# Kernel tuning notes

Hardware: AMD Instinct MI355X
Metric: run time of the kernel (lower is better)

Reference implementation:

```python
import jax, jax.numpy as jnp
import numpy as np

B, N, C, H = 4, 1024, 1024, 16
D = C // H  # head_dim = 64
SCALE = D ** -0.5


def setup_inputs() -> dict:
    key = jax.random.key(0)
    ks = jax.random.split(key, 7)
    std = 0.02
    return {
        "xq": jax.random.normal(ks[0], (B, N, C), dtype=jnp.float32),
        "xk": jax.random.normal(ks[1], (B, N, C), dtype=jnp.float32),
        "xv": jax.random.normal(ks[2], (B, N, C), dtype=jnp.float32),
        # torch nn.Linear weights are [out_features, in_features]
        "Wq": jax.random.normal(ks[3], (C, C), dtype=jnp.float32) * std,
        "Wkv": jax.random.normal(ks[4], (2 * C, C), dtype=jnp.float32) * std,
        "Wp": jax.random.normal(ks[5], (C, C), dtype=jnp.float32) * std,
        "bp": jax.random.normal(ks[6], (C,), dtype=jnp.float32) * std,
    }


def reference(xq, xk, xv, Wq, Wkv, Wp, bp):
    b, nq, c = xq.shape
    nk = xk.shape[1]
    # q projection -> [B, H, Nq, D]
    q = (xq @ Wq.T).reshape(b, nq, H, D).transpose(0, 2, 1, 3)
    # HPA: shared projection produces K and V from xk (xv unused)
    kv = xk @ Wkv.T  # [B, Nk, 2C]
    k, v = jnp.split(kv, 2, axis=-1)
    k = k.reshape(b, nk, H, D).transpose(0, 2, 1, 3)  # [B, H, Nk, D]
    v = v.reshape(b, nk, H, D).transpose(0, 2, 1, 3)  # [B, H, Nk, D]
    # pre-softmax scores (attn_save in original)
    attn = jnp.einsum("bhqd,bhkd->bhqk", q, k) * SCALE  # [B, H, Nq, Nk]
    p = jax.nn.softmax(attn, axis=-1)
    x = jnp.einsum("bhqk,bhkd->bhqd", p, v)  # [B, H, Nq, D]
    x = x.transpose(0, 2, 1, 3).reshape(b, nq, c)
    x = x @ Wp.T + bp
    # returns (x transposed to [Nq, B, C], mean-over-heads pre-softmax scores)
    return x.transpose(1, 0, 2), attn.sum(axis=1) / H
```

## Files before the change

kernel.cpp:

```cpp
#include <hip/hip_runtime.h>
#include <hip/hip_bf16.h>
#include <stdint.h>

typedef __attribute__((ext_vector_type(8))) short bf16x8;
typedef __attribute__((ext_vector_type(4))) float f32x4;

#define B_DIM 4
#define N_DIM 1024
#define C_DIM 1024
#define NT 16

#define QSCALE 0.18033688011112042f
#define OUT1_ALPHA 0.04332169878499658f

__device__ __forceinline__ ushort f2bf(float f) {
  union { float f; uint32_t u; } v; v.f = f;
  uint32_t r = (v.u + 0x7FFFu + ((v.u >> 16) & 1u)) >> 16;
  return (ushort)r;
}

__device__ __forceinline__ uint32_t cvtpk(float lo, float hi) {
  uint32_t r;
  asm("v_cvt_pk_bf16_f32 %0, %1, %2" : "=v"(r) : "v"(lo), "v"(hi));
  return r;
}

__device__ __forceinline__ void gload_lds16(const void* g, void* l) {
  __builtin_amdgcn_global_load_lds(
      (const __attribute__((address_space(1))) void*)g,
      (__attribute__((address_space(3))) void*)l, 16, 0, 0);
}

__device__ __forceinline__ f32x4 mfma16(bf16x8 a, bf16x8 b, f32x4 c) {
  return __builtin_amdgcn_mfma_f32_16x16x32_bf16(a, b, c, 0, 0, 0);
}

__global__ __launch_bounds__(256) void cvt_all(
    const float* __restrict__ xq, const float* __restrict__ xk,
    const float* __restrict__ Wq, const float* __restrict__ Wkv,
    const float* __restrict__ Wp, ushort* __restrict__ xq_b,
    ushort* __restrict__ xk_b, ushort* __restrict__ Wq_b,
    ushort* __restrict__ Wkv_b, ushort* __restrict__ Wp_b) {
  int bid = blockIdx.x;
  const float* s;
  ushort* d;
  int off;
  if (bid < 4096) { s = xq; d = xq_b; off = bid; }
  else if (bid < 8192) { s = xk; d = xk_b; off = bid - 4096; }
  else if (bid < 9216) { s = Wq; d = Wq_b; off = bid - 8192; }
  else if (bid < 11264) { s = Wkv; d = Wkv_b; off = bid - 9216; }
  else { s = Wp; d = Wp_b; off = bid - 11264; }
  int i = off * 1024 + threadIdx.x * 4;
  float4 v = *(const float4*)(s + i);
  ushort4 o;
  o.x = f2bf(v.x); o.y = f2bf(v.y); o.z = f2bf(v.z); o.w = f2bf(v.w);
  *(ushort4*)(d + i) = o;
}

template <int MODE, int BN>
__device__ __forceinline__ void gemm_core(
    ushort* As, ushort* Bs, const ushort* A, const ushort* Bm, float* Cf,
    ushort* Cb, int K, int lda, int ldb, int ldc, int m0, int n0, float alpha,
    const float* bias) {
  constexpr int MR = (BN == 128) ? 4 : 2;
  constexpr int WM = (BN == 128) ? 64 : 32;
  constexpr int BBUF = BN * 32;
  const int tid = threadIdx.x;
  const int l = tid & 63, wv = tid >> 6, lg = l >> 4, lr = l & 15;
  const int wr = (BN == 128) ? (wv >> 1) : wv;
  const int wc = (BN == 128) ? (wv & 1) : 0;
  const int r0 = tid >> 2, c0 = (tid & 3) * 8;
  const int wb = (tid & ~63) * 8;
  const ushort* Arow0 = A + (size_t)(m0 + r0) * lda + c0;
  const ushort* Arow1 = A + (size_t)(m0 + 64 + r0) * lda + c0;
  const ushort* Brow0 = Bm + (size_t)(n0 + r0) * ldb + c0;
  const ushort* Brow1 =
      (BN == 128) ? (Bm + (size_t)(n0 + 64 + r0) * ldb + c0) : Brow0;

  gload_lds16(Arow0, As + wb);
  gload_lds16(Arow1, As + 2048 + wb);
  gload_lds16(Brow0, Bs + wb);
  if (BN == 128) gload_lds16(Brow1, Bs + 2048 + wb);
  f32x4 acc[MR][4] = {};
  __syncthreads();
  const int nk = K >> 5;
  for (int t = 0; t < nk; ++t) {
    const int pA = (t & 1) ? 4096 : 0;
    const int pB = (t & 1) ? BBUF : 0;
    if (t + 1 < nk) {
      const int nA = pA ^ 4096, nB = pB ^ BBUF;
      const int k0 = (t + 1) << 5;
      gload_lds16(Arow0 + k0, As + nA + wb);
      gload_lds16(Arow1 + k0, As + nA + 2048 + wb);
      gload_lds16(Brow0 + k0, Bs + nB + wb);
      if (BN == 128) gload_lds16(Brow1 + k0, Bs + nB + 2048 + wb);
    }
    bf16x8 af[MR], bfr[4];
#pragma unroll
    for (int m = 0; m < MR; m++)
      af[m] = *(const bf16x8*)&As[pA + (wr * WM + m * 16 + lr) * 32 + lg * 8];
#pragma unroll
    for (int n = 0; n < 4; n++)
      bfr[n] = *(const bf16x8*)&Bs[pB + (wc * 64 + n * 16 + lr) * 32 + lg * 8];
#pragma unroll
    for (int m = 0; m < MR; m++)
#pragma unroll
      for (int n = 0; n < 4; n++)
        acc[m][n] = mfma16(af[m], bfr[n], acc[m][n]);
    __syncthreads();
  }

#pragma unroll
  for (int m = 0; m < MR; m++) {
    const int row = m0 + wr * WM + m * 16 + lg * 4;
#pragma unroll
    for (int n = 0; n < 4; n++) {
      const int col = n0 + wc * 64 + n * 16 + lr;
#pragma unroll
      for (int r = 0; r < 4; r++) {
        float v = acc[m][n][r];
        if (MODE == 0) {
          Cb[(size_t)(row + r) * ldc + col] = f2bf(v * alpha);
        } else if (MODE == 1) {
          Cf[(size_t)(row + r) * ldc + col] = v * alpha;
        } else {
          int gm = row + r;
          int bb = gm >> 10, nq = gm & 1023;
          Cf[((size_t)nq * B_DIM + bb) * C_DIM + col] = v + bias[col];
        }
      }
    }
  }
}

template <int MODE, int BN>
__global__ __launch_bounds__(256) void gemm_bt(
    const ushort* __restrict__ A, const ushort* __restrict__ Bm,
    float* __restrict__ Cf, ushort* __restrict__ Cb, int K, int lda, int ldb,
    int ldc, long sA, long sB, long sC, float alpha,
    const float* __restrict__ bias) {
  __shared__ ushort As[2 * 4096];
  __shared__ ushort Bs[2 * BN * 32];
  const int z = blockIdx.z;
  float* cf = (MODE == 0) ? nullptr : (Cf + (size_t)z * sC);
  ushort* cb = (MODE == 0) ? (Cb + (size_t)z * sC) : nullptr;
  gemm_core<MODE, BN>(As, Bs, A + (size_t)z * sA, Bm + (size_t)z * sB, cf, cb,
                      K, lda, ldb, ldc, blockIdx.y * 128, blockIdx.x * BN,
                      alpha, bias);
}

__global__ __launch_bounds__(256) void gemm_dual(
    const ushort* __restrict__ A0, const ushort* __restrict__ B0,
    ushort* __restrict__ C0, const ushort* __restrict__ A1,
    const ushort* __restrict__ B1, ushort* __restrict__ C1) {
  __shared__ ushort As[2 * 4096];
  __shared__ ushort Bs[2 * 4096];
  int bid = blockIdx.x;
  if (bid < 256) {
    gemm_core<0, 128>(As, Bs, A0, B0, nullptr, C0, 1024, 1024, 1024, 1024,
                      (bid >> 3) * 128, (bid & 7) * 128, QSCALE, nullptr);
  } else {
    bid -= 256;
    gemm_core<0, 128>(As, Bs, A1, B1, nullptr, C1, 1024, 1024, 1024, 2048,
                      (bid >> 4) * 128, (bid & 15) * 128, 1.f, nullptr);
  }
}

__device__ __forceinline__ void writeVt(ushort* dst, uint4 a, uint4 b, int vr,
                                        int cb) {
  union { uint4 q[2]; ushort u[16]; } x;
  x.q[0] = a; x.q[1] = b;
  const int kc = vr >> 3, ki = vr & 7;
#pragma unroll
  for (int j = 0; j < 16; j++) {
    int d = cb + j;
    int sd = (d & 7) ^ ((d >> 3) & 7);
    dst[d * 64 + ((kc ^ sd) << 3) + ki] = x.u[j];
  }
}

__global__ __launch_bounds__(256) void flash_out1(
    const ushort* __restrict__ Qp, const ushort* __restrict__ KVp,
    ushort* __restrict__ O, float* __restrict__ out1) {
  __shared__ ushort sm[5 * 4096];
  int bid = blockIdx.x;

  if (bid >= 1024) {
    int b2 = bid - 1024;
    int z = b2 >> 7;
    gemm_core<1, 64>(sm, sm + 8192, Qp + (size_t)z * 1048576,
                     KVp + (size_t)z * 2097152, out1 + (size_t)z * 1048576,
                     nullptr, 1024, 1024, 2048, 1024, ((b2 >> 4) & 7) * 128,
                     (b2 & 15) * 64, OUT1_ALPHA, nullptr);
    return;
  }

  ushort* Ks0 = sm;
  ushort* Vt0 = sm + 8192;
  ushort* QPs = sm + 16384;

  const int tid = threadIdx.x;
  const int w = tid >> 6, l = tid & 63;
  const int lg = l >> 4, lr = l & 15, lr7 = lr & 7;
  const int bh = bid >> 4;
  const int b = bh >> 4, h = bh & 15;
  const int q0 = (bid & 15) * 64;

  const ushort* Qg =
      Qp + (size_t)b * (N_DIM * C_DIM) + (size_t)q0 * C_DIM + h * 64;
  const ushort* Kg = KVp + (size_t)b * (N_DIM * 2 * C_DIM) + h * 64;
  const ushort* Vg = Kg + C_DIM;

  const int sr = tid >> 3;
  const int sc = (tid & 7) ^ (sr & 7);
  const int wb = (tid & ~63) * 8;
  const int vr = tid >> 2, cb2 = (tid & 3) * 16;

  gload_lds16(Qg + (size_t)sr * C_DIM + sc * 8, QPs + wb);
  gload_lds16(Qg + (size_t)(32 + sr) * C_DIM + sc * 8, QPs + 2048 + wb);
  gload_lds16(Kg + (size_t)sr * 2048 + sc * 8, Ks0 + wb);
  gload_lds16(Kg + (size_t)(32 + sr) * 2048 + sc * 8, Ks0 + 2048 + wb);
  const ushort* vsrc = Vg + (size_t)vr * 2048 + cb2;
  uint4 rv0 = *(const uint4*)vsrc;
  uint4 rv1 = *(const uint4*)(vsrc + 8);
  __syncthreads();
  writeVt(Vt0, rv0, rv1, vr, cb2);
  const int qrow = w * 16 + lr;
  bf16x8 qa0 = *(const bf16x8*)&QPs[qrow * 64 + ((lg ^ (qrow & 7)) << 3)];
  bf16x8 qa1 = *(const bf16x8*)&QPs[qrow * 64 + (((lg + 4) ^ (qrow & 7)) << 3)];
  __syncthreads();

  f32x4 oacc[4] = {};
  float lp = 0.f;
  char* Pwb = (char*)(QPs + w * 1024);

  uint4 nv0, nv1;
  for (int t = 0; t < NT; ++t) {
    const int cur = t & 1;
    ushort* Kc = Ks0 + cur * 4096;
    ushort* Vc = Vt0 + cur * 4096;
    if (t + 1 < NT) {
      const int kt2 = (t + 1) * 64;
      ushort* Kn = Ks0 + (cur ^ 1) * 4096;
      gload_lds16(Kg + (size_t)(kt2 + sr) * 2048 + sc * 8, Kn + wb);
      gload_lds16(Kg + (size_t)(kt2 + 32 + sr) * 2048 + sc * 8, Kn + 2048 + wb);
      const ushort* nsrc = Vg + (size_t)(kt2 + vr) * 2048 + cb2;
      nv0 = *(const uint4*)nsrc;
      nv1 = *(const uint4*)(nsrc + 8);
    }

    f32x4 s[4];
    __builtin_amdgcn_s_setprio(1);
#pragma unroll
    for (int kf = 0; kf < 4; kf++) {
      const int krow = kf * 16 + lr;
      bf16x8 kb0 = *(const bf16x8*)&Kc[krow * 64 + ((lg ^ (krow & 7)) << 3)];
      bf16x8 kb1 =
          *(const bf16x8*)&Kc[krow * 64 + (((lg + 4) ^ (krow & 7)) << 3)];
      f32x4 zz = {};
      zz = mfma16(kb0, qa0, zz);
      zz = mfma16(kb1, qa1, zz);
      s[kf] = zz;
    }
    __builtin_amdgcn_s_setprio(0);

#pragma unroll
    for (int kf = 0; kf < 4; kf++)
#pragma unroll
      for (int r = 0; r < 4; r++) {
        float p = exp2f(s[kf][r]);
        s[kf][r] = p;
        lp += p;
      }

#pragma unroll
    for (int kf = 0; kf < 4; kf++) {
      uint32_t w0 = cvtpk(s[kf][0], s[kf][1]);
      uint32_t w1 = cvtpk(s[kf][2], s[kf][3]);
      int woff = lr * 128 + ((((kf << 1) | (lg >> 1)) ^ lr7) << 4) +
                 ((lg & 1) << 3);
      *(uint2*)(Pwb + woff) = make_uint2(w0, w1);
    }
    asm volatile("s_waitcnt lgkmcnt(0)" ::: "memory");
    __builtin_amdgcn_sched_barrier(0);
    bf16x8 pa0 = *(const bf16x8*)(Pwb + lr * 128 + ((lg ^ lr7) << 4));
    bf16x8 pa1 = *(const bf16x8*)(Pwb + lr * 128 + (((lg + 4) ^ lr7) << 4));

    __builtin_amdgcn_s_setprio(1);
#pragma unroll
    for (int df = 0; df < 4; df++) {
      const int drow = df * 16 + lr;
      const int sd = (drow & 7) ^ ((drow >> 3) & 7);
      bf16x8 vb0 = *(const bf16x8*)&Vc[drow * 64 + ((lg ^ sd) << 3)];
      bf16x8 vb1 = *(const bf16x8*)&Vc[drow * 64 + (((lg + 4) ^ sd) << 3)];
      oacc[df] = mfma16(pa0, vb0, oacc[df]);
      oacc[df] = mfma16(pa1, vb1, oacc[df]);
    }
    __builtin_amdgcn_s_setprio(0);

    if (t + 1 < NT) {
      writeVt(Vt0 + (cur ^ 1) * 4096, nv0, nv1, vr, cb2);
      __syncthreads();
    }
  }

  lp += __shfl_xor(lp, 16);
  lp += __shfl_xor(lp, 32);
  float linv[4];
#pragma unroll
  for (int r = 0; r < 4; r++) linv[r] = 1.0f / __shfl(lp, lg * 4 + r);

  ushort* Og = O + (size_t)b * (N_DIM * C_DIM) +
               (size_t)(q0 + w * 16 + lg * 4) * C_DIM + h * 64;
#pragma unroll
  for (int df = 0; df < 4; df++)
#pragma unroll
    for (int r = 0; r < 4; r++)
      Og[(size_t)r * C_DIM + df * 16 + lr] = f2bf(oacc[df][r] * linv[r]);
}

extern "C" void kernel_launch(void* const* d_in, const int* in_sizes, int n_in,
                              void* d_out, int out_size, void* d_ws,
                              size_t ws_size, hipStream_t stream) {
  const float* xq = (const float*)d_in[0];
  const float* xk = (const float*)d_in[1];
  const float* Wq = (const float*)d_in[3];
  const float* Wkv = (const float*)d_in[4];
  const float* Wp = (const float*)d_in[5];
  const float* bp = (const float*)d_in[6];

  ushort* ws = (ushort*)d_ws;
  ushort* xq_b = ws;
  ushort* xk_b = xq_b + 4194304;
  ushort* Wq_b = xk_b + 4194304;
  ushort* Wkv_b = Wq_b + 1048576;
  ushort* Wp_b = Wkv_b + 2097152;
  ushort* Qp = Wp_b + 1048576;
  ushort* KVp = Qp + 4194304;
  ushort* Ob = KVp + 8388608;

  float* out0 = (float*)d_out;
  float* out1 = out0 + 4194304;

  cvt_all<<<12288, 256, 0, stream>>>(xq, xk, Wq, Wkv, Wp, xq_b, xk_b, Wq_b,
                                     Wkv_b, Wp_b);
  gemm_dual<<<768, 256, 0, stream>>>(xq_b, Wq_b, Qp, xk_b, Wkv_b, KVp);
  flash_out1<<<1536, 256, 0, stream>>>(Qp, KVp, Ob, out1);
  gemm_bt<2, 64><<<dim3(16, 32, 1), 256, 0, stream>>>(
      Ob, Wp_b, out0, nullptr, 1024, 1024, 1024, 1024, 0, 0, 0, 1.f, bp);
}
```

Baseline: 219.9 us.

## Triple-buffer GEMM loads and use transposed LDS reads for V in flash attention

The shared GEMM core moves from double to triple buffering, prefetching two K-tiles ahead. It replaces the per-iteration __syncthreads with a partial vmcnt wait plus barrier and swizzles the LDS columns to avoid bank conflicts. The flash attention kernel stops transposing V through registers with scalar LDS stores. It now loads V directly into LDS with global_load_lds and reads it with ds_read_b64_tr_b16, keeping P in registers for 16x16x16 MFMAs instead of round-tripping P through LDS. This uses more LDS per block and adds inline-asm scheduling constraints that may reduce occupancy or limit overlap.

Result: faster. 213.8 us (-2.8%).

```diff
diff --git a/kernel.cpp b/kernel.cpp
--- a/kernel.cpp
+++ b/kernel.cpp
@@ -3,6 +3,7 @@
 #include <stdint.h>
 
 typedef __attribute__((ext_vector_type(8))) short bf16x8;
+typedef __attribute__((ext_vector_type(4))) short bf16x4;
 typedef __attribute__((ext_vector_type(4))) float f32x4;
 
 #define B_DIM 4
@@ -33,6 +34,15 @@
 
 __device__ __forceinline__ f32x4 mfma16(bf16x8 a, bf16x8 b, f32x4 c) {
   return __builtin_amdgcn_mfma_f32_16x16x32_bf16(a, b, c, 0, 0, 0);
+}
+
+__device__ __forceinline__ void mfma16x16(bf16x4 a, bf16x4 b, f32x4& c) {
+  asm("v_mfma_f32_16x16x16_bf16 %0, %1, %2, %0" : "+v"(c) : "v"(a), "v"(b));
+}
+
+template <int N>
+__device__ __forceinline__ void waitcnt_vm() {
+  asm volatile("s_waitcnt vmcnt(%0)" ::"i"(N) : "memory");
 }
 
 __global__ __launch_bounds__(256) void cvt_all(
@@ -64,51 +74,67 @@
     const float* bias) {
   constexpr int MR = (BN == 128) ? 4 : 2;
   constexpr int WM = (BN == 128) ? 64 : 32;
-  constexpr int BBUF = BN * 32;
+  constexpr int ABUF = 4096, BBUF = BN * 32;
+  constexpr int NLD = (BN == 128) ? 4 : 3;
   const int tid = threadIdx.x;
   const int l = tid & 63, wv = tid >> 6, lg = l >> 4, lr = l & 15;
   const int wr = (BN == 128) ? (wv >> 1) : wv;
   const int wc = (BN == 128) ? (wv & 1) : 0;
-  const int r0 = tid >> 2, c0 = (tid & 3) * 8;
+  const int r0 = tid >> 2;
+  const int cs = ((tid & 3) ^ ((r0 >> 1) & 3)) * 8;
   const int wb = (tid & ~63) * 8;
-  const ushort* Arow0 = A + (size_t)(m0 + r0) * lda + c0;
-  const ushort* Arow1 = A + (size_t)(m0 + 64 + r0) * lda + c0;
-  const ushort* Brow0 = Bm + (size_t)(n0 + r0) * ldb + c0;
-  const ushort* Brow1 =
-      (BN == 128) ? (Bm + (size_t)(n0 + 64 + r0) * ldb + c0) : Brow0;
-
-  gload_lds16(Arow0, As + wb);
-  gload_lds16(Arow1, As + 2048 + wb);
-  gload_lds16(Brow0, Bs + wb);
-  if (BN == 128) gload_lds16(Brow1, Bs + 2048 + wb);
+  const int cA = ((lg ^ ((lr >> 1) & 3)) << 3);
+  const ushort* Ar0 = A + (size_t)(m0 + r0) * lda + cs;
+  const ushort* Ar1 = A + (size_t)(m0 + 64 + r0) * lda + cs;
+  const ushort* Br0 = Bm + (size_t)(n0 + r0) * ldb + cs;
+  const ushort* Br1 = Bm + (size_t)(n0 + 64 + r0) * ldb + cs;
+
+#define STAGE(t, bi)                                                     \
+  {                                                                      \
+    const int k0_ = (t) << 5;                                            \
+    gload_lds16(Ar0 + k0_, As + (bi) * ABUF + wb);                       \
+    gload_lds16(Ar1 + k0_, As + (bi) * ABUF + 2048 + wb);                \
+    gload_lds16(Br0 + k0_, Bs + (bi) * BBUF + wb);                       \
+    if (BN == 128) gload_lds16(Br1 + k0_, Bs + (bi) * BBUF + 2048 + wb); \
+  }
+
+  const int nk = K >> 5;
+  STAGE(0, 0);
+  STAGE(1, 1);
   f32x4 acc[MR][4] = {};
-  __syncthreads();
-  const int nk = K >> 5;
+  waitcnt_vm<NLD>();
+  __builtin_amdgcn_sched_barrier(0);
+  __builtin_amdgcn_s_barrier();
+  __builtin_amdgcn_sched_barrier(0);
+  int b0 = 0;
   for (int t = 0; t < nk; ++t) {
-    const int pA = (t & 1) ? 4096 : 0;
-    const int pB = (t & 1) ? BBUF : 0;
-    if (t + 1 < nk) {
-      const int nA = pA ^ 4096, nB = pB ^ BBUF;
-      const int k0 = (t + 1) << 5;
-      gload_lds16(Arow0 + k0, As + nA + wb);
-      gload_lds16(Arow1 + k0, As + nA + 2048 + wb);
-      gload_lds16(Brow0 + k0, Bs + nB + wb);
-      if (BN == 128) gload_lds16(Brow1 + k0, Bs + nB + 2048 + wb);
-    }
+    const int b2 = (b0 + 2 >= 3) ? b0 - 1 : b0 + 2;
+    if (t + 2 < nk) STAGE(t + 2, b2);
+    const ushort* Ab = As + b0 * ABUF;
+    const ushort* Bb = Bs + b0 * BBUF;
     bf16x8 af[MR], bfr[4];
 #pragma unroll
     for (int m = 0; m < MR; m++)
-      af[m] = *(const bf16x8*)&As[pA + (wr * WM + m * 16 + lr) * 32 + lg * 8];
+      af[m] = *(const bf16x8*)&Ab[(wr * WM + m * 16 + lr) * 32 + cA];
 #pragma unroll
     for (int n = 0; n < 4; n++)
-      bfr[n] = *(const bf16x8*)&Bs[pB + (wc * 64 + n * 16 + lr) * 32 + lg * 8];
+      bfr[n] = *(const bf16x8*)&Bb[(wc * 64 + n * 16 + lr) * 32 + cA];
+    __builtin_amdgcn_s_setprio(1);
 #pragma unroll
     for (int m = 0; m < MR; m++)
 #pragma unroll
       for (int n = 0; n < 4; n++)
         acc[m][n] = mfma16(af[m], bfr[n], acc[m][n]);
-    __syncthreads();
-  }
+    __builtin_amdgcn_s_setprio(0);
+    if (t + 1 < nk) {
+      if (t + 2 < nk) waitcnt_vm<NLD>(); else waitcnt_vm<0>();
+      __builtin_amdgcn_sched_barrier(0);
+      __builtin_amdgcn_s_barrier();
+      __builtin_amdgcn_sched_barrier(0);
+    }
+    b0 = (b0 + 1 >= 3) ? 0 : b0 + 1;
+  }
+#undef STAGE
 
 #pragma unroll
   for (int m = 0; m < MR; m++) {
@@ -139,8 +165,8 @@
     float* __restrict__ Cf, ushort* __restrict__ Cb, int K, int lda, int ldb,
     int ldc, long sA, long sB, long sC, float alpha,
     const float* __restrict__ bias) {
-  __shared__ ushort As[2 * 4096];
-  __shared__ ushort Bs[2 * BN * 32];
+  __shared__ ushort As[3 * 4096];
+  __shared__ ushort Bs[3 * BN * 32];
   const int z = blockIdx.z;
   float* cf = (MODE == 0) ? nullptr : (Cf + (size_t)z * sC);
   ushort* cb = (MODE == 0) ? (Cb + (size_t)z * sC) : nullptr;
@@ -153,8 +179,8 @@
     const ushort* __restrict__ A0, const ushort* __restrict__ B0,
     ushort* __restrict__ C0, const ushort* __restrict__ A1,
     const ushort* __restrict__ B1, ushort* __restrict__ C1) {
-  __shared__ ushort As[2 * 4096];
-  __shared__ ushort Bs[2 * 4096];
+  __shared__ ushort As[3 * 4096];
+  __shared__ ushort Bs[3 * 4096];
   int bid = blockIdx.x;
   if (bid < 256) {
     gemm_core<0, 128>(As, Bs, A0, B0, nullptr, C0, 1024, 1024, 1024, 1024,
@@ -166,29 +192,16 @@
   }
 }
 
-__device__ __forceinline__ void writeVt(ushort* dst, uint4 a, uint4 b, int vr,
-                                        int cb) {
-  union { uint4 q[2]; ushort u[16]; } x;
-  x.q[0] = a; x.q[1] = b;
-  const int kc = vr >> 3, ki = vr & 7;
-#pragma unroll
-  for (int j = 0; j < 16; j++) {
-    int d = cb + j;
-    int sd = (d & 7) ^ ((d >> 3) & 7);
-    dst[d * 64 + ((kc ^ sd) << 3) + ki] = x.u[j];
-  }
-}
-
 __global__ __launch_bounds__(256) void flash_out1(
     const ushort* __restrict__ Qp, const ushort* __restrict__ KVp,
     ushort* __restrict__ O, float* __restrict__ out1) {
-  __shared__ ushort sm[5 * 4096];
+  __shared__ ushort sm[20480];
   int bid = blockIdx.x;
 
   if (bid >= 1024) {
     int b2 = bid - 1024;
     int z = b2 >> 7;
-    gemm_core<1, 64>(sm, sm + 8192, Qp + (size_t)z * 1048576,
+    gemm_core<1, 64>(sm, sm + 12288, Qp + (size_t)z * 1048576,
                      KVp + (size_t)z * 2097152, out1 + (size_t)z * 1048576,
                      nullptr, 1024, 1024, 2048, 1024, ((b2 >> 4) & 7) * 128,
                      (b2 & 15) * 64, OUT1_ALPHA, nullptr);
@@ -196,12 +209,12 @@
   }
 
   ushort* Ks0 = sm;
-  ushort* Vt0 = sm + 8192;
-  ushort* QPs = sm + 16384;
+  ushort* Vs0 = sm + 8192;
+  ushort* Qs = sm + 16384;
 
   const int tid = threadIdx.x;
   const int w = tid >> 6, l = tid & 63;
-  const int lg = l >> 4, lr = l & 15, lr7 = lr & 7;
+  const int lg = l >> 4, lr = l & 15;
   const int bh = bid >> 4;
   const int b = bh >> 4, h = bh & 15;
   const int q0 = (bid & 15) * 64;
@@ -214,39 +227,45 @@
   const int sr = tid >> 3;
   const int sc = (tid & 7) ^ (sr & 7);
   const int wb = (tid & ~63) * 8;
-  const int vr = tid >> 2, cb2 = (tid & 3) * 16;
-
-  gload_lds16(Qg + (size_t)sr * C_DIM + sc * 8, QPs + wb);
-  gload_lds16(Qg + (size_t)(32 + sr) * C_DIM + sc * 8, QPs + 2048 + wb);
-  gload_lds16(Kg + (size_t)sr * 2048 + sc * 8, Ks0 + wb);
-  gload_lds16(Kg + (size_t)(32 + sr) * 2048 + sc * 8, Ks0 + 2048 + wb);
-  const ushort* vsrc = Vg + (size_t)vr * 2048 + cb2;
-  uint4 rv0 = *(const uint4*)vsrc;
-  uint4 rv1 = *(const uint4*)(vsrc + 8);
+  const int vrow = (l & 31) >> 1;
+  const int vdc = ((l >> 5) << 4) + (l & 1) * 8;
+
+#define STAGE_K(kt2, buf)                                                   \
+  {                                                                         \
+    gload_lds16(Kg + (size_t)((kt2) + sr) * 2048 + sc * 8, (buf) + wb);     \
+    gload_lds16(Kg + (size_t)((kt2) + 32 + sr) * 2048 + sc * 8,             \
+                (buf) + 2048 + wb);                                         \
+  }
+#define STAGE_V(kt2, buf)                                                   \
+  {                                                                         \
+    gload_lds16(Vg + (size_t)((kt2) + w * 16 + vrow) * 2048 + vdc,          \
+                (buf) + (w * 4 + 0) * 256);                                 \
+    gload_lds16(Vg + (size_t)((kt2) + w * 16 + vrow) * 2048 + 32 + vdc,     \
+                (buf) + (w * 4 + 2) * 256);                                 \
+  }
+
+  gload_lds16(Qg + (size_t)sr * C_DIM + sc * 8, Qs + wb);
+  gload_lds16(Qg + (size_t)(32 + sr) * C_DIM + sc * 8, Qs + 2048 + wb);
+  STAGE_K(0, Ks0);
+  STAGE_V(0, Vs0);
   __syncthreads();
-  writeVt(Vt0, rv0, rv1, vr, cb2);
   const int qrow = w * 16 + lr;
-  bf16x8 qa0 = *(const bf16x8*)&QPs[qrow * 64 + ((lg ^ (qrow & 7)) << 3)];
-  bf16x8 qa1 = *(const bf16x8*)&QPs[qrow * 64 + (((lg + 4) ^ (qrow & 7)) << 3)];
-  __syncthreads();
+  bf16x8 qa0 = *(const bf16x8*)&Qs[qrow * 64 + ((lg ^ (qrow & 7)) << 3)];
+  bf16x8 qa1 = *(const bf16x8*)&Qs[qrow * 64 + (((lg + 4) ^ (qrow & 7)) << 3)];
 
   f32x4 oacc[4] = {};
   float lp = 0.f;
-  char* Pwb = (char*)(QPs + w * 1024);
-
-  uint4 nv0, nv1;
+  const uint32_t vbase =
+      (uint32_t)(uintptr_t)(__attribute__((address_space(3))) ushort*)Vs0 +
+      (uint32_t)(l * 8);
+
   for (int t = 0; t < NT; ++t) {
     const int cur = t & 1;
     ushort* Kc = Ks0 + cur * 4096;
-    ushort* Vc = Vt0 + cur * 4096;
     if (t + 1 < NT) {
       const int kt2 = (t + 1) * 64;
-      ushort* Kn = Ks0 + (cur ^ 1) * 4096;
-      gload_lds16(Kg + (size_t)(kt2 + sr) * 2048 + sc * 8, Kn + wb);
-      gload_lds16(Kg + (size_t)(kt2 + 32 + sr) * 2048 + sc * 8, Kn + 2048 + wb);
-      const ushort* nsrc = Vg + (size_t)(kt2 + vr) * 2048 + cb2;
-      nv0 = *(const uint4*)nsrc;
-      nv1 = *(const uint4*)(nsrc + 8);
+      STAGE_K(kt2, Ks0 + (cur ^ 1) * 4096);
+      STAGE_V(kt2, Vs0 + (cur ^ 1) * 4096);
     }
 
     f32x4 s[4];
@@ -264,45 +283,49 @@
     }
     __builtin_amdgcn_s_setprio(0);
 
-#pragma unroll
-    for (int kf = 0; kf < 4; kf++)
-#pragma unroll
-      for (int r = 0; r < 4; r++) {
-        float p = exp2f(s[kf][r]);
-        s[kf][r] = p;
-        lp += p;
-      }
-
+    bf16x4 pa[4];
 #pragma unroll
     for (int kf = 0; kf < 4; kf++) {
-      uint32_t w0 = cvtpk(s[kf][0], s[kf][1]);
-      uint32_t w1 = cvtpk(s[kf][2], s[kf][3]);
-      int woff = lr * 128 + ((((kf << 1) | (lg >> 1)) ^ lr7) << 4) +
-                 ((lg & 1) << 3);
-      *(uint2*)(Pwb + woff) = make_uint2(w0, w1);
-    }
-    asm volatile("s_waitcnt lgkmcnt(0)" ::: "memory");
-    __builtin_amdgcn_sched_barrier(0);
-    bf16x8 pa0 = *(const bf16x8*)(Pwb + lr * 128 + ((lg ^ lr7) << 4));
-    bf16x8 pa1 = *(const bf16x8*)(Pwb + lr * 128 + (((lg + 4) ^ lr7) << 4));
-
+      float p0 = exp2f(s[kf][0]), p1 = exp2f(s[kf][1]);
+      float p2 = exp2f(s[kf][2]), p3 = exp2f(s[kf][3]);
+      lp += (p0 + p1) + (p2 + p3);
+      union { uint32_t u[2]; bf16x4 v; } pk;
+      pk.u[0] = cvtpk(p0, p1);
+      pk.u[1] = cvtpk(p2, p3);
+      pa[kf] = pk.v;
+    }
+
+    const uint32_t trb = vbase + cur * 8192;
     __builtin_amdgcn_s_setprio(1);
-#pragma unroll
-    for (int df = 0; df < 4; df++) {
-      const int drow = df * 16 + lr;
-      const int sd = (drow & 7) ^ ((drow >> 3) & 7);
-      bf16x8 vb0 = *(const bf16x8*)&Vc[drow * 64 + ((lg ^ sd) << 3)];
-      bf16x8 vb1 = *(const bf16x8*)&Vc[drow * 64 + (((lg + 4) ^ sd) << 3)];
-      oacc[df] = mfma16(pa0, vb0, oacc[df]);
-      oacc[df] = mfma16(pa1, vb1, oacc[df]);
-    }
+#define PV_DF(df, O0, O1, O2, O3)                                          \
+  {                                                                        \
+    bf16x4 v0, v1, v2, v3;                                                 \
+    asm volatile("ds_read_b64_tr_b16 %0, %1 offset:" #O0                   \
+                 : "=v"(v0) : "v"(trb));                                   \
+    asm volatile("ds_read_b64_tr_b16 %0, %1 offset:" #O1                   \
+                 : "=v"(v1) : "v"(trb));                                   \
+    asm volatile("ds_read_b64_tr_b16 %0, %1 offset:" #O2                   \
+                 : "=v"(v2) : "v"(trb));                                   \
+    asm volatile("ds_read_b64_tr_b16 %0, %1 offset:" #O3                   \
+                 : "=v"(v3) : "v"(trb));                                   \
+    asm volatile("s_waitcnt lgkmcnt(0)" ::: "memory");                     \
+    __builtin_amdgcn_sched_barrier(0);                                     \
+    mfma16x16(pa[0], v0, oacc[df]);                                        \
+    mfma16x16(pa[1], v1, oacc[df]);                                        \
+    mfma16x16(pa[2], v2, oacc[df]);                                        \
+    mfma16x16(pa[3], v3, oacc[df]);                                        \
+  }
+    PV_DF(0, 0, 2048, 4096, 6144)
+    PV_DF(1, 512, 2560, 4608, 6656)
+    PV_DF(2, 1024, 3072, 5120, 7168)
+    PV_DF(3, 1536, 3584, 5632, 7680)
+#undef PV_DF
     __builtin_amdgcn_s_setprio(0);
 
-    if (t + 1 < NT) {
-      writeVt(Vt0 + (cur ^ 1) * 4096, nv0, nv1, vr, cb2);
-      __syncthreads();
-    }
-  }
+    __syncthreads();
+  }
+#undef STAGE_K
+#undef STAGE_V
 
   lp += __shfl_xor(lp, 16);
   lp += __shfl_xor(lp, 32);
```
